# Kernel optimization log

Measured on AMD Instinct MI355X. Metric: run time of the kernel, lower is better.

Reference implementation:

```python
import jax, jax.numpy as jnp
import numpy as np

B, N, D = 16, 2048, 256  # batch (pairs*2), num_keypoints, descriptor_dim


def setup_inputs() -> dict:
    key = jax.random.key(0)
    k1, k2, k3, k4 = jax.random.split(key, 4)
    descriptors = jax.random.normal(k1, (B, N, D), dtype=jnp.float32)
    mask = jax.random.randint(k2, (B, N), 0, 2, dtype=jnp.int32)
    proj_w = jax.random.normal(k3, (D, D), dtype=jnp.float32) * 0.02
    proj_b = jnp.zeros((D,), dtype=jnp.float32)
    match_w = jax.random.normal(k4, (1, D), dtype=jnp.float32) * 0.02
    match_b = jnp.zeros((1,), dtype=jnp.float32)
    return {"descriptors": descriptors, "mask": mask, "proj_w": proj_w,
            "proj_b": proj_b, "match_w": match_w, "match_b": match_b}


def reference(descriptors, mask, proj_w, proj_b, match_w, match_b):
    batch, n, d = descriptors.shape
    pairs = batch // 2
    # final projection + temperature scaling
    m_desc = (descriptors @ proj_w.T + proj_b) / jnp.asarray(d, descriptors.dtype) ** 0.25
    m_desc = m_desc.reshape(pairs, 2, n, d)
    # similarity: [pairs, n0, n1]
    similarity = jnp.einsum('bnd,bmd->bnm', m_desc[:, 0], m_desc[:, 1])
    mask_p = mask.reshape(pairs, 2, n)
    pair_mask = mask_p[:, 0][:, :, None] * mask_p[:, 1][:, None, :]
    neg_min = jnp.finfo(similarity.dtype).min
    similarity = jnp.where(pair_mask == 0, neg_min, similarity)
    # matchability logits: [B, n, 1] -> split per pair
    matchability = (descriptors @ match_w.T + match_b).reshape(pairs, 2, n)
    m0 = matchability[:, 0]  # [pairs, n]
    m1 = matchability[:, 1]  # [pairs, n]
    certainties = jax.nn.log_sigmoid(m0)[:, :, None] + jax.nn.log_sigmoid(m1)[:, None, :]
    scores0 = jax.nn.log_softmax(similarity, axis=2)
    scores1 = jax.nn.log_softmax(similarity, axis=1)
    inner = scores0 + scores1 + certainties
    scores = jnp.zeros((pairs, n + 1, n + 1), dtype=similarity.dtype)
    scores = scores.at[:, :n, :n].set(inner)
    scores = scores.at[:, :-1, -1].set(jax.nn.log_sigmoid(-m0))
    scores = scores.at[:, -1, :-1].set(jax.nn.log_sigmoid(-m1))
    return scores
```

## Files before the change

### kernel.cpp

```cpp
#include <hip/hip_runtime.h>
#include <math.h>

typedef unsigned short u16;
typedef __attribute__((ext_vector_type(8))) short bf16x8;
typedef __attribute__((ext_vector_type(4))) float f32x4;

#define N 2048
#define D 256
#define PAIRS 8
#define NO 2049
#define NEGMIN  -3.40282347e38f
#define MASKVAL -3.0e38f
#define LDA 72
#define LDST 136

#define WS_LS0   0
#define WS_LS1   (1*PAIRS*N)
#define WS_LSN0  (2*PAIRS*N)
#define WS_LSN1  (3*PAIRS*N)
#define WS_RMAX  (4*PAIRS*N)
#define WS_RLSE  (5*PAIRS*N)
#define WS_CMAX  (6*PAIRS*N)
#define WS_CLSE  (7*PAIRS*N)
#define WS_RPM   (8*PAIRS*N)
#define WS_RPS   (WS_RPM + PAIRS*16*N)
#define WS_CPM   (WS_RPS + PAIRS*16*N)
#define WS_CPS   (WS_CPM + PAIRS*16*N)
#define WS_F_COUNT (WS_CPS + PAIRS*16*N)

__device__ __forceinline__ float b2f(u16 u) {
    return __uint_as_float(((unsigned)u) << 16);
}
__device__ __forceinline__ u16 f2b(float f) {
    unsigned x = __float_as_uint(f);
    x += 0x7FFFu + ((x >> 16) & 1u);
    return (u16)(x >> 16);
}
__device__ __forceinline__ unsigned pk2(float a, float b) {
    return (unsigned)f2b(a) | ((unsigned)f2b(b) << 16);
}
__device__ __forceinline__ float logsig(float x) {
    return fminf(x, 0.f) - log1pf(expf(-fabsf(x)));
}
__device__ __forceinline__ void online1(float& m, float& s, float x) {
    float nm = fmaxf(m, x);
    float e = __expf(fminf(m, x) - nm);
    s = (x > m) ? s * e + 1.f : s + e;
    m = nm;
}
__device__ __forceinline__ void onmerge(float& m, float& s, float om, float os) {
    float nm = fmaxf(m, om);
    s = s * __expf(m - nm) + os * __expf(om - nm);
    m = nm;
}
__device__ __forceinline__ void gl_lds16(const u16* g, u16* l) {
    __builtin_amdgcn_global_load_lds(
        (const __attribute__((address_space(1))) unsigned*)(const void*)g,
        (__attribute__((address_space(3))) unsigned*)(void*)l, 16, 0, 0);
}

__global__ __launch_bounds__(256) void k_proj_mfma(const float* __restrict__ A,
                                                   const float* __restrict__ W,
                                                   const float* __restrict__ bias,
                                                   const float* __restrict__ mw,
                                                   const float* __restrict__ mb,
                                                   u16* __restrict__ mdesc,
                                                   float* __restrict__ wsf) {
    __shared__ union {
        struct { u16 A[128 * LDA]; u16 B[128 * LDA]; } t;
        u16 stage[128][LDST];
    } sh;
    int r0 = blockIdx.x * 128, c0 = blockIdx.y * 128;
    int tid = threadIdx.x;
    int w = tid >> 6, lane = tid & 63;
    int ln = lane & 15, q = lane >> 4;
    int wr0 = (w >> 1) * 64, wc0 = (w & 1) * 64;
    f32x4 zero = {0.f, 0.f, 0.f, 0.f};
    f32x4 acc[4][4];
    #pragma unroll
    for (int a = 0; a < 4; ++a)
        #pragma unroll
        for (int b = 0; b < 4; ++b) acc[a][b] = zero;
    float mdot[4] = {0.f, 0.f, 0.f, 0.f};
    int domatch = (blockIdx.y == 0);

    for (int kb = 0; kb < D; kb += 64) {
        __syncthreads();
        #pragma unroll
        for (int t = 0; t < 4; ++t) {
            int c = t * 256 + tid;
            int row = c >> 3, part = c & 7;
            const float* ap = A + (size_t)(r0 + row) * D + kb + part * 8;
            float4 f0 = *(const float4*)ap;
            float4 f1 = *(const float4*)(ap + 4);
            uint4 va;
            va.x = pk2(f0.x, f0.y); va.y = pk2(f0.z, f0.w);
            va.z = pk2(f1.x, f1.y); va.w = pk2(f1.z, f1.w);
            *(uint4*)&sh.t.A[row * LDA + part * 8] = va;
            if (domatch) {
                float4 w0 = *(const float4*)(mw + kb + part * 8);
                float4 w1 = *(const float4*)(mw + kb + part * 8 + 4);
                mdot[t] += f0.x*w0.x + f0.y*w0.y + f0.z*w0.z + f0.w*w0.w
                         + f1.x*w1.x + f1.y*w1.y + f1.z*w1.z + f1.w*w1.w;
            }
            const float* bp = W + (size_t)(c0 + row) * D + kb + part * 8;
            float4 g0 = *(const float4*)bp;
            float4 g1 = *(const float4*)(bp + 4);
            uint4 vb;
            vb.x = pk2(g0.x, g0.y); vb.y = pk2(g0.z, g0.w);
            vb.z = pk2(g1.x, g1.y); vb.w = pk2(g1.z, g1.w);
            *(uint4*)&sh.t.B[row * LDA + part * 8] = vb;
        }
        __syncthreads();
        #pragma unroll
        for (int kk = 0; kk < 64; kk += 32) {
            bf16x8 af[4], bf[4];
            #pragma unroll
            for (int ri = 0; ri < 4; ++ri)
                af[ri] = *(const bf16x8*)&sh.t.A[(wr0 + ri*16 + ln) * LDA + kk + q*8];
            #pragma unroll
            for (int ci = 0; ci < 4; ++ci)
                bf[ci] = *(const bf16x8*)&sh.t.B[(wc0 + ci*16 + ln) * LDA + kk + q*8];
            #pragma unroll
            for (int ri = 0; ri < 4; ++ri)
                #pragma unroll
                for (int ci = 0; ci < 4; ++ci)
                    acc[ri][ci] = __builtin_amdgcn_mfma_f32_16x16x32_bf16(af[ri], bf[ci], acc[ri][ci], 0, 0, 0);
        }
    }
    if (domatch) {
        #pragma unroll
        for (int t = 0; t < 4; ++t) {
            float s = mdot[t];
            s += __shfl_xor(s, 1, 64);
            s += __shfl_xor(s, 2, 64);
            s += __shfl_xor(s, 4, 64);
            if ((tid & 7) == 0) {
                int row_g = r0 + t * 32 + (tid >> 3);
                float m = s + mb[0];
                int b = row_g >> 11;
                int i = row_g & (N - 1);
                int pp = b >> 1, sid = b & 1;
                float ls = logsig(m), lsn = logsig(-m);
                if (sid == 0) { wsf[WS_LS0 + pp*N + i] = ls; wsf[WS_LSN0 + pp*N + i] = lsn; }
                else          { wsf[WS_LS1 + pp*N + i] = ls; wsf[WS_LSN1 + pp*N + i] = lsn; }
            }
        }
    }
    __syncthreads();
    #pragma unroll
    for (int ri = 0; ri < 4; ++ri) {
        #pragma unroll
        for (int reg = 0; reg < 4; ++reg) {
            int row_l = wr0 + ri*16 + q*4 + reg;
            #pragma unroll
            for (int ci = 0; ci < 4; ++ci) {
                int col = c0 + wc0 + ci*16 + ln;
                float v = (acc[ri][ci][reg] + bias[col]) * 0.25f;
                sh.stage[row_l][wc0 + ci*16 + ln] = f2b(v);
            }
        }
    }
    __syncthreads();
    {
        int row_l = tid >> 1, half = tid & 1;
        u16* dp = mdesc + (size_t)(r0 + row_l) * D + c0 + half * 64;
        const u16* lp = &sh.stage[row_l][half * 64];
        #pragma unroll
        for (int i = 0; i < 8; ++i)
            *(uint4*)(dp + i * 8) = *(const uint4*)(lp + i * 8);
    }
}

__global__ __launch_bounds__(256) void k_sim_mfma(const u16* __restrict__ mdesc,
                                                  const int* __restrict__ mask,
                                                  u16* __restrict__ sim,
                                                  float* __restrict__ wsf) {
    __shared__ union {
        struct { u16 A[128 * 64]; u16 B[128 * 64]; } t;
        u16 stage[128][LDST];
    } sh;
    __shared__ float rpm[128][2], rps[128][2];
    __shared__ float cpm[128][2], cps[128][2];
    int p = blockIdx.z;
    const u16* Am = mdesc + (size_t)(2*p) * N * D;
    const u16* Bm = mdesc + (size_t)(2*p + 1) * N * D;
    int r0 = blockIdx.x * 128, c0 = blockIdx.y * 128;
    int tid = threadIdx.x;
    int w = tid >> 6, lane = tid & 63;
    int ln = lane & 15, q = lane >> 4;
    int wr0 = (w >> 1) * 64, wc0 = (w & 1) * 64;
    int rsub = lane >> 3;
    int scol = (((lane & 7) ^ rsub) << 3);
    f32x4 zero = {0.f, 0.f, 0.f, 0.f};
    f32x4 acc[4][4];
    #pragma unroll
    for (int a = 0; a < 4; ++a)
        #pragma unroll
        for (int b = 0; b < 4; ++b) acc[a][b] = zero;

    for (int kb = 0; kb < D; kb += 64) {
        #pragma unroll
        for (int j = 0; j < 4; ++j) {
            int row = w * 32 + j * 8 + rsub;
            gl_lds16(Am + (size_t)(r0 + row) * D + kb + scol, &sh.t.A[(w * 32 + j * 8) * 64]);
            gl_lds16(Bm + (size_t)(c0 + row) * D + kb + scol, &sh.t.B[(w * 32 + j * 8) * 64]);
        }
        __syncthreads();
        #pragma unroll
        for (int kk = 0; kk < 64; kk += 32) {
            bf16x8 af[4], bf[4];
            int cbase = kk * 2 + q * 16;
            int cswz = cbase ^ ((ln & 7) << 4);
            #pragma unroll
            for (int ri = 0; ri < 4; ++ri) {
                int row = wr0 + ri*16 + ln;
                af[ri] = *(const bf16x8*)((const char*)sh.t.A + row * 128 + cswz);
            }
            #pragma unroll
            for (int ci = 0; ci < 4; ++ci) {
                int row = wc0 + ci*16 + ln;
                bf[ci] = *(const bf16x8*)((const char*)sh.t.B + row * 128 + cswz);
            }
            #pragma unroll
            for (int ri = 0; ri < 4; ++ri)
                #pragma unroll
                for (int ci = 0; ci < 4; ++ci)
                    acc[ri][ci] = __builtin_amdgcn_mfma_f32_16x16x32_bf16(af[ri], bf[ci], acc[ri][ci], 0, 0, 0);
        }
        __syncthreads();
    }
    const int* m0 = mask + (size_t)(2*p) * N;
    const int* m1 = mask + (size_t)(2*p + 1) * N;
    int mcol[4];
    #pragma unroll
    for (int ci = 0; ci < 4; ++ci) mcol[ci] = m1[c0 + wc0 + ci*16 + ln];
    #pragma unroll
    for (int ri = 0; ri < 4; ++ri) {
        #pragma unroll
        for (int reg = 0; reg < 4; ++reg) {
            int row_l = wr0 + ri*16 + q*4 + reg;
            int mr = m0[r0 + row_l];
            #pragma unroll
            for (int ci = 0; ci < 4; ++ci) {
                float v = (mr && mcol[ci]) ? acc[ri][ci][reg] : MASKVAL;
                acc[ri][ci][reg] = v;
                sh.stage[row_l][wc0 + ci*16 + ln] = f2b(v);
            }
        }
    }
    #pragma unroll
    for (int ri = 0; ri < 4; ++ri) {
        #pragma unroll
        for (int reg = 0; reg < 4; ++reg) {
            float m = acc[ri][0][reg], s = 1.f;
            online1(m, s, acc[ri][1][reg]);
            online1(m, s, acc[ri][2][reg]);
            online1(m, s, acc[ri][3][reg]);
            #pragma unroll
            for (int off = 1; off <= 8; off <<= 1) {
                float om = __shfl_xor(m, off, 64);
                float os = __shfl_xor(s, off, 64);
                onmerge(m, s, om, os);
            }
            if (ln == 0) {
                int rl = wr0 + ri*16 + q*4 + reg;
                rpm[rl][w & 1] = m; rps[rl][w & 1] = s;
            }
        }
    }
    #pragma unroll
    for (int ci = 0; ci < 4; ++ci) {
        float m = acc[0][ci][0], s = 1.f;
        #pragma unroll
        for (int ri = 0; ri < 4; ++ri)
            #pragma unroll
            for (int reg = 0; reg < 4; ++reg)
                if (!(ri == 0 && reg == 0)) online1(m, s, acc[ri][ci][reg]);
        #pragma unroll
        for (int off = 16; off <= 32; off <<= 1) {
            float om = __shfl_xor(m, off, 64);
            float os = __shfl_xor(s, off, 64);
            onmerge(m, s, om, os);
        }
        if (q == 0) {
            int cl = wc0 + ci*16 + ln;
            cpm[cl][w >> 1] = m; cps[cl][w >> 1] = s;
        }
    }
    __syncthreads();
    {
        int row_l = tid >> 1, half = tid & 1;
        u16* sp = sim + ((size_t)p * N + r0 + row_l) * N + c0 + half * 64;
        const u16* lp = &sh.stage[row_l][half * 64];
        #pragma unroll
        for (int i = 0; i < 8; ++i)
            *(uint4*)(sp + i * 8) = *(const uint4*)(lp + i * 8);
    }
    if (tid < 128) {
        float m = rpm[tid][0], s = rps[tid][0];
        onmerge(m, s, rpm[tid][1], rps[tid][1]);
        size_t o = (size_t)(p * 16 + blockIdx.y) * N + r0 + tid;
        wsf[WS_RPM + o] = m; wsf[WS_RPS + o] = s;
    } else {
        int c = tid - 128;
        float m = cpm[c][0], s = cps[c][0];
        onmerge(m, s, cpm[c][1], cps[c][1]);
        size_t o = (size_t)(p * 16 + blockIdx.x) * N + c0 + c;
        wsf[WS_CPM + o] = m;
        wsf[WS_CPS + o] = s;
    }
}

__global__ __launch_bounds__(256) void k_red(float* __restrict__ wsf) {
    int i = blockIdx.x * 256 + threadIdx.x;
    int p = blockIdx.y;
    float m = wsf[WS_CPM + (size_t)(p*16) * N + i];
    float s = wsf[WS_CPS + (size_t)(p*16) * N + i];
    #pragma unroll
    for (int rb = 1; rb < 16; ++rb)
        onmerge(m, s, wsf[WS_CPM + (size_t)(p*16 + rb) * N + i],
                      wsf[WS_CPS + (size_t)(p*16 + rb) * N + i]);
    wsf[WS_CMAX + p * N + i] = m;
    wsf[WS_CLSE + p * N + i] = logf(s);
}

__global__ __launch_bounds__(256) void k_final(u16* __restrict__ out,
                                               const u16* __restrict__ sim,
                                               const float* __restrict__ wsf) {
    int strip = blockIdx.x;
    int p = blockIdx.y;
    int tid = threadIdx.x;
    __shared__ float rm_l[8], rl_l[8], l0_l[8], ln0_l[8];
    if (tid < 128) {
        int r = tid >> 4, cb = tid & 15;
        int i = strip * 8 + r;
        if (i < N) {
            float m = wsf[WS_RPM + (size_t)(p*16 + cb) * N + i];
            float sv = wsf[WS_RPS + (size_t)(p*16 + cb) * N + i];
            #pragma unroll
            for (int off = 1; off <= 8; off <<= 1) {
                float om = __shfl_xor(m, off, 64);
                float os = __shfl_xor(sv, off, 64);
                onmerge(m, sv, om, os);
            }
            if (cb == 0) {
                rm_l[r]  = m;
                rl_l[r]  = logf(sv);
                l0_l[r]  = wsf[WS_LS0  + p*N + i];
                ln0_l[r] = wsf[WS_LSN0 + p*N + i];
            }
        }
    }
    __syncthreads();
    unsigned* up = (unsigned*)out;
    #pragma unroll
    for (int k = 0; k < 4; ++k) {
        int kk = k * 256 + tid;
        int jc = 2 * kk;
        float cm0 = wsf[WS_CMAX + p*N + jc];
        float cl0 = wsf[WS_CLSE + p*N + jc];
        float s10 = wsf[WS_LS1  + p*N + jc];
        float cm1 = wsf[WS_CMAX + p*N + jc + 1];
        float cl1 = wsf[WS_CLSE + p*N + jc + 1];
        float s11 = wsf[WS_LS1  + p*N + jc + 1];
        float cm2 = 0.f, cl2 = 0.f, s12 = 0.f;
        if (jc + 2 < N) {
            cm2 = wsf[WS_CMAX + p*N + jc + 2];
            cl2 = wsf[WS_CLSE + p*N + jc + 2];
            s12 = wsf[WS_LS1  + p*N + jc + 2];
        }
        for (int r = 0; r < 8; ++r) {
            int i = strip * 8 + r;
            if (i > N) break;
            size_t B0 = ((size_t)p * NO + i) * NO;
            int head = (p + i) & 1;
            size_t U0 = (B0 + head) >> 1;
            if (i == N) {
                int j0 = 2*kk + head;
                float o0 = (j0 < N) ? wsf[WS_LSN1 + p*N + j0] : 0.f;
                int j1 = j0 + 1;
                float o1 = (j1 < N) ? wsf[WS_LSN1 + p*N + j1] : 0.f;
                up[U0 + kk] = pk2(o0, o1);
                if (tid == 0 && k == 0) {
                    if (head) out[B0] = f2b(wsf[WS_LSN1 + p*N]);
                    else      out[B0 + N] = 0;
                }
                continue;
            }
            float rm = rm_l[r], rl = rl_l[r], l0 = l0_l[r], ln0 = ln0_l[r];
            const u16* srow = sim + ((size_t)p * N + i) * N;
            unsigned a = *(const unsigned*)(srow + jc);
            float o0, o1;
            if (head) {
                float x0 = b2f((u16)(a >> 16));
                float a0 = (x0 - rm) - rl;
                float b0 = (x0 - cm1) - cl1;
                o0 = fmaxf(fmaxf(a0 + b0, MASKVAL) + (l0 + s11), MASKVAL);
                if (jc + 2 < N) {
                    float x1 = b2f(srow[jc + 2]);
                    float a1 = (x1 - rm) - rl;
                    float b1 = (x1 - cm2) - cl2;
                    o1 = fmaxf(fmaxf(a1 + b1, MASKVAL) + (l0 + s12), MASKVAL);
                } else {
                    o1 = ln0;
                }
            } else {
                float x0 = b2f((u16)a);
                float a0 = (x0 - rm) - rl;
                float b0 = (x0 - cm0) - cl0;
                o0 = fmaxf(fmaxf(a0 + b0, MASKVAL) + (l0 + s10), MASKVAL);
                float x1 = b2f((u16)(a >> 16));
                float a1 = (x1 - rm) - rl;
                float b1 = (x1 - cm1) - cl1;
                o1 = fmaxf(fmaxf(a1 + b1, MASKVAL) + (l0 + s11), MASKVAL);
            }
            up[U0 + kk] = pk2(o0, o1);
            if (tid == 0 && k == 0) {
                if (head) {
                    float x = b2f(srow[0]);
                    float aa = (x - rm) - rl;
                    float bb = (x - wsf[WS_CMAX + p*N]) - wsf[WS_CLSE + p*N];
                    out[B0] = f2b(fmaxf(fmaxf(aa + bb, MASKVAL) + (l0 + wsf[WS_LS1 + p*N]), MASKVAL));
                } else {
                    out[B0 + N] = f2b(ln0);
                }
            }
        }
    }
}

extern "C" void kernel_launch(void* const* d_in, const int* in_sizes, int n_in,
                              void* d_out, int out_size, void* d_ws, size_t ws_size,
                              hipStream_t stream) {
    const float* desc    = (const float*)d_in[0];
    const int*   mask    = (const int*)d_in[1];
    const float* proj_w  = (const float*)d_in[2];
    const float* proj_b  = (const float*)d_in[3];
    const float* match_w = (const float*)d_in[4];
    const float* match_b = (const float*)d_in[5];
    u16*   out = (u16*)d_out;
    float* wsf = (float*)d_ws;
    u16*   mdesc = (u16*)((char*)d_ws + (size_t)WS_F_COUNT * sizeof(float));
    u16*   simw  = mdesc + (size_t)16 * N * D;

    k_proj_mfma<<<dim3(256, 2),    256, 0, stream>>>(desc, proj_w, proj_b, match_w, match_b, mdesc, wsf);
    k_sim_mfma <<<dim3(16, 16, 8), 256, 0, stream>>>(mdesc, mask, simw, wsf);
    k_red      <<<dim3(8, 8),      256, 0, stream>>>(wsf);
    k_final    <<<dim3(257, 8),    256, 0, stream>>>(out, simw, wsf);
}
```

Baseline: 275.7 us.

## Double-buffer K-loop LDS tiles and use two-pass max/sum-exp epilogue

The similarity GEMM kernel now keeps two LDS buffers per operand and issues the global-to-LDS loads for the next 64-wide K slice before computing on the current one. This is meant to overlap memory latency with MFMA work. The per-tile row and column log-sum-exp reductions now find the max first and then sum the exponentials, instead of running an online max/sum merge at every step. That removes exp-rescale operations and halves the shuffle payload, but it doubles the LDS footprint of the operand tiles, which may lower occupancy.

```diff
diff --git a/kernel.cpp b/kernel.cpp
--- a/kernel.cpp
+++ b/kernel.cpp
@@ -177,7 +177,7 @@
                                                   u16* __restrict__ sim,
                                                   float* __restrict__ wsf) {
     __shared__ union {
-        struct { u16 A[128 * 64]; u16 B[128 * 64]; } t;
+        u16 lds[4][128 * 64];
         u16 stage[128][LDST];
     } sh;
     __shared__ float rpm[128][2], rps[128][2];
@@ -199,14 +199,28 @@
         #pragma unroll
         for (int b = 0; b < 4; ++b) acc[a][b] = zero;
 
-    for (int kb = 0; kb < D; kb += 64) {
-        #pragma unroll
-        for (int j = 0; j < 4; ++j) {
-            int row = w * 32 + j * 8 + rsub;
-            gl_lds16(Am + (size_t)(r0 + row) * D + kb + scol, &sh.t.A[(w * 32 + j * 8) * 64]);
-            gl_lds16(Bm + (size_t)(c0 + row) * D + kb + scol, &sh.t.B[(w * 32 + j * 8) * 64]);
-        }
-        __syncthreads();
+    #define STAGE(t_, bufi_) do {                                               \
+        int kb_ = (t_) * 64;                                                    \
+        u16* Ad_ = &sh.lds[(bufi_)*2][0];                                       \
+        u16* Bd_ = &sh.lds[(bufi_)*2+1][0];                                     \
+        _Pragma("unroll")                                                       \
+        for (int j_ = 0; j_ < 4; ++j_) {                                        \
+            int row_ = w * 32 + j_ * 8 + rsub;                                  \
+            gl_lds16(Am + (size_t)(r0 + row_) * D + kb_ + scol,                 \
+                     Ad_ + (w * 32 + j_ * 8) * 64);                             \
+            gl_lds16(Bm + (size_t)(c0 + row_) * D + kb_ + scol,                 \
+                     Bd_ + (w * 32 + j_ * 8) * 64);                             \
+        }                                                                       \
+    } while (0)
+
+    STAGE(0, 0);
+    __syncthreads();
+    #pragma unroll
+    for (int t = 0; t < 4; ++t) {
+        int cur = t & 1;
+        if (t < 3) STAGE(t + 1, cur ^ 1);
+        const char* Abase = (const char*)&sh.lds[cur*2][0];
+        const char* Bbase = (const char*)&sh.lds[cur*2+1][0];
         #pragma unroll
         for (int kk = 0; kk < 64; kk += 32) {
             bf16x8 af[4], bf[4];
@@ -215,12 +229,12 @@
             #pragma unroll
             for (int ri = 0; ri < 4; ++ri) {
                 int row = wr0 + ri*16 + ln;
-                af[ri] = *(const bf16x8*)((const char*)sh.t.A + row * 128 + cswz);
+                af[ri] = *(const bf16x8*)(Abase + row * 128 + cswz);
             }
             #pragma unroll
             for (int ci = 0; ci < 4; ++ci) {
                 int row = wc0 + ci*16 + ln;
-                bf[ci] = *(const bf16x8*)((const char*)sh.t.B + row * 128 + cswz);
+                bf[ci] = *(const bf16x8*)(Bbase + row * 128 + cswz);
             }
             #pragma unroll
             for (int ri = 0; ri < 4; ++ri)
@@ -230,6 +244,8 @@
         }
         __syncthreads();
     }
+    #undef STAGE
+
     const int* m0 = mask + (size_t)(2*p) * N;
     const int* m1 = mask + (size_t)(2*p + 1) * N;
     int mcol[4];
@@ -253,16 +269,16 @@
     for (int ri = 0; ri < 4; ++ri) {
         #pragma unroll
         for (int reg = 0; reg < 4; ++reg) {
-            float m = acc[ri][0][reg], s = 1.f;
-            online1(m, s, acc[ri][1][reg]);
-            online1(m, s, acc[ri][2][reg]);
-            online1(m, s, acc[ri][3][reg]);
-            #pragma unroll
-            for (int off = 1; off <= 8; off <<= 1) {
-                float om = __shfl_xor(m, off, 64);
-                float os = __shfl_xor(s, off, 64);
-                onmerge(m, s, om, os);
-            }
+            float x0 = acc[ri][0][reg], x1 = acc[ri][1][reg];
+            float x2 = acc[ri][2][reg], x3 = acc[ri][3][reg];
+            float m = fmaxf(fmaxf(x0, x1), fmaxf(x2, x3));
+            #pragma unroll
+            for (int off = 1; off <= 8; off <<= 1)
+                m = fmaxf(m, __shfl_xor(m, off, 64));
+            float s = __expf(x0 - m) + __expf(x1 - m) + __expf(x2 - m) + __expf(x3 - m);
+            #pragma unroll
+            for (int off = 1; off <= 8; off <<= 1)
+                s += __shfl_xor(s, off, 64);
             if (ln == 0) {
                 int rl = wr0 + ri*16 + q*4 + reg;
                 rpm[rl][w & 1] = m; rps[rl][w & 1] = s;
@@ -271,18 +287,24 @@
     }
     #pragma unroll
     for (int ci = 0; ci < 4; ++ci) {
-        float m = acc[0][ci][0], s = 1.f;
+        float m = acc[0][ci][0];
         #pragma unroll
         for (int ri = 0; ri < 4; ++ri)
             #pragma unroll
             for (int reg = 0; reg < 4; ++reg)
-                if (!(ri == 0 && reg == 0)) online1(m, s, acc[ri][ci][reg]);
-        #pragma unroll
-        for (int off = 16; off <= 32; off <<= 1) {
-            float om = __shfl_xor(m, off, 64);
-            float os = __shfl_xor(s, off, 64);
-            onmerge(m, s, om, os);
-        }
+                if (!(ri == 0 && reg == 0)) m = fmaxf(m, acc[ri][ci][reg]);
+        #pragma unroll
+        for (int off = 16; off <= 32; off <<= 1)
+            m = fmaxf(m, __shfl_xor(m, off, 64));
+        float s = 0.f;
+        #pragma unroll
+        for (int ri = 0; ri < 4; ++ri)
+            #pragma unroll
+            for (int reg = 0; reg < 4; ++reg)
+                s += __expf(acc[ri][ci][reg] - m);
+        #pragma unroll
+        for (int off = 16; off <= 32; off <<= 1)
+            s += __shfl_xor(s, off, 64);
         if (q == 0) {
             int cl = wc0 + ci*16 + ln;
             cpm[cl][w >> 1] = m; cps[cl][w >> 1] = s;
```

Measured after the change: 275.9 us. About the same (+0.1%).
